# Performance work log

Hardware: AMD Instinct MI355X
Metric: run time of the kernel (lower is better)

Reference implementation:

```python
import jax, jax.numpy as jnp
import numpy as np

B, L, D, H, M = 2, 512, 1024, 16, 16384
HD = D // H  # 64


def setup_inputs() -> dict:
    key = jax.random.key(0)
    ks = jax.random.split(key, 8)
    s = 0.02
    return {
        "x": jax.random.normal(ks[0], (B, L, D), dtype=jnp.float32),
        "mem_keys": jax.random.normal(ks[1], (M, HD), dtype=jnp.float32),
        "mem_values": jax.random.normal(ks[2], (M, HD), dtype=jnp.float32),
        "Wq": jax.random.normal(ks[3], (D, D), dtype=jnp.float32) * s,
        "bq": jnp.zeros((D,), jnp.float32),
        "Wk": jax.random.normal(ks[4], (D, D), dtype=jnp.float32) * s,
        "bk": jnp.zeros((D,), jnp.float32),
        "Wv": jax.random.normal(ks[5], (D, D), dtype=jnp.float32) * s,
        "bv": jnp.zeros((D,), jnp.float32),
        "Wo": jax.random.normal(ks[6], (D, D), dtype=jnp.float32) * s,
        "bo": jnp.zeros((D,), jnp.float32),
        "top_k": 8,
    }


def reference(x, mem_keys, mem_values, Wq, bq, Wk, bk, Wv, bv, Wo, bo, top_k):
    b, l, d = x.shape
    h, hd = H, d // H
    # Q/K/V projections -> [B, L, H, HD]
    q = (x @ Wq.T + bq).reshape(b, l, h, hd)
    k = (x @ Wk.T + bk).reshape(b, l, h, hd)
    v = (x @ Wv.T + bv).reshape(b, l, h, hd)

    # exact inner-product top-k memory search (FAISS equivalent) per (b, l, h) query
    q_flat = q.reshape(b * l * h, hd)
    sim = q_flat @ mem_keys.T                      # [B*L*H, M]
    idx = jax.lax.top_k(sim, top_k)[1]             # [B*L*H, K]
    # gather retrieved KV, lay out as memory-prefix along seq: [B, L*K, H, HD]
    m_k = mem_keys[idx].reshape(b, l, h, top_k, hd).transpose(0, 1, 3, 2, 4).reshape(b, l * top_k, h, hd)
    m_v = mem_values[idx].reshape(b, l, h, top_k, hd).transpose(0, 1, 3, 2, 4).reshape(b, l * top_k, h, hd)

    k_full = jnp.concatenate([m_k, k], axis=1)     # [B, Lm+L, H, HD]
    v_full = jnp.concatenate([m_v, v], axis=1)
    lm = l * top_k

    scale = 1.0 / np.sqrt(hd)
    scores = jnp.einsum("blhd,bmhd->bhlm", q, k_full) * scale
    # memory prefix always visible; local part causal (flash_attn bottom-right causal)
    i = jnp.arange(l)[:, None]
    j = jnp.arange(lm + l)[None, :]
    mask = (j < lm) | ((j - lm) <= i)              # [L, Lm+L]
    neg = jnp.finfo(scores.dtype).min
    attn = jax.nn.softmax(jnp.where(mask, scores, neg), axis=-1)
    out = jnp.einsum("bhlm,bmhd->blhd", attn, v_full).reshape(b, l, d)
    return out @ Wo.T + bo
```

## Files before the change

kernel.cpp:

```cpp
#include <hip/hip_runtime.h>

typedef __bf16 bf16_t;
typedef __bf16 bf16x8 __attribute__((ext_vector_type(8)));
typedef __bf16 bf16x4 __attribute__((ext_vector_type(4)));
typedef __bf16 bf16x2 __attribute__((ext_vector_type(2)));
typedef float f32x4 __attribute__((ext_vector_type(4)));

#define DEV __device__ __forceinline__
#define MFMA16 __builtin_amdgcn_mfma_f32_16x16x32_bf16

constexpr int Bb = 2, Ls = 512, Dd = 1024, Hh = 16, HD = 64, Mm = 16384, TK = 8;
constexpr int KSPLIT = 4;
constexpr int CAP = 40;
constexpr int NQ = Bb * Ls * Hh;
constexpr int CH = 3;

constexpr size_t OFF_QF   = 0;
constexpr size_t OFF_KH2  = OFF_QF + (size_t)NQ * HD;
constexpr size_t OFF_KL2  = OFF_KH2 + (size_t)NQ * HD / 2;
constexpr size_t OFF_VH2  = OFF_KL2 + (size_t)NQ * HD / 2;
constexpr size_t OFF_VL2  = OFF_VH2 + (size_t)NQ * HD / 2;
constexpr size_t OFF_QH   = OFF_VL2 + (size_t)NQ * HD / 2;
constexpr size_t OFF_QL   = OFF_QH + (size_t)NQ * HD / 2;
constexpr size_t OFF_KHG  = OFF_QL + (size_t)NQ * HD / 2;
constexpr size_t OFF_FCAND = OFF_KHG + (size_t)Mm * HD / 2;
constexpr size_t OFF_FCNT  = OFF_FCAND + (size_t)KSPLIT * NQ * CAP;
constexpr size_t OFF_F8   = OFF_FCNT + (size_t)KSPLIT * NQ;
constexpr size_t OFF_ML   = OFF_F8 + (size_t)NQ * TK;
constexpr size_t OFF_PA   = OFF_ML + (size_t)CH * NQ * 2;
constexpr size_t WS_ELEMS = OFF_PA + (size_t)CH * NQ * HD + 16;
constexpr size_t WS_BYTES = WS_ELEMS * 4;

constexpr size_t OFF_GKL = OFF_FCAND;
constexpr size_t OFF_GVH = OFF_GKL + (size_t)Mm * HD / 2;
constexpr size_t OFF_GVL = OFF_GVH + (size_t)Mm * HD / 2;
static_assert(OFF_GVL + (size_t)Mm * HD / 2 <= OFF_FCNT, "alias fits in FCAND");

DEV void ld8f(const float* p, float* dst) {
  float4 a = *(const float4*)p, b = *(const float4*)(p + 4);
  dst[0]=a.x; dst[1]=a.y; dst[2]=a.z; dst[3]=a.w;
  dst[4]=b.x; dst[5]=b.y; dst[6]=b.z; dst[7]=b.w;
}

DEV void split8(const float* av, bf16x8& hi, bf16x8& lo) {
#pragma unroll
  for (int j = 0; j < 8; ++j) {
    bf16_t h_ = (bf16_t)av[j];
    hi[j] = h_;
    lo[j] = (bf16_t)(av[j] - (float)h_);
  }
}

DEV bf16x8 ld8h(const bf16_t* p) {
  bf16x4 a = *(const bf16x4*)p;
  bf16x4 b = *(const bf16x4*)(p + 4);
  bf16x8 r;
#pragma unroll
  for (int i = 0; i < 4; ++i) { r[i] = a[i]; r[i + 4] = b[i]; }
  return r;
}

__global__ __launch_bounds__(256) void ws_sentinel(float* __restrict__ out, int n, float v) {
  int i = blockIdx.x * 256 + threadIdx.x;
  if (i < n) out[i] = v;
}

__global__ __launch_bounds__(256) void prep_keys(const float* __restrict__ mk,
                                                 bf16_t* __restrict__ khg) {
  const size_t i = ((size_t)blockIdx.x * 256 + threadIdx.x) * 8;
  float v[8]; ld8f(mk + i, v);
  bf16x8 h;
#pragma unroll
  for (int j = 0; j < 8; ++j) h[j] = (bf16_t)v[j];
  *(bf16x8*)(khg + i) = h;
}

__global__ __launch_bounds__(256) void prep_kv2(const float* __restrict__ mk,
                                                const float* __restrict__ mv,
                                                bf16_t* __restrict__ gkl,
                                                bf16_t* __restrict__ gvh,
                                                bf16_t* __restrict__ gvl) {
  const size_t i = ((size_t)blockIdx.x * 256 + threadIdx.x) * 8;
  float a[8]; ld8f(mk + i, a);
  float b[8]; ld8f(mv + i, b);
  bf16x8 kl, vh, vl;
#pragma unroll
  for (int j = 0; j < 8; ++j) {
    bf16_t kh_ = (bf16_t)a[j];
    kl[j] = (bf16_t)(a[j] - (float)kh_);
    bf16_t vh_ = (bf16_t)b[j];
    vh[j] = vh_;
    vl[j] = (bf16_t)(b[j] - (float)vh_);
  }
  *(bf16x8*)(gkl + i) = kl;
  *(bf16x8*)(gvh + i) = vh;
  *(bf16x8*)(gvl + i) = vl;
}

__global__ __launch_bounds__(256) void qkv_mfma(
    const float* __restrict__ x,
    const float* __restrict__ Wq, const float* __restrict__ bq,
    const float* __restrict__ Wk, const float* __restrict__ bk,
    const float* __restrict__ Wv, const float* __restrict__ bv,
    float* __restrict__ qf, bf16_t* __restrict__ qhp, bf16_t* __restrict__ qlp,
    bf16_t* __restrict__ kh2, bf16_t* __restrict__ kl2,
    bf16_t* __restrict__ vh2, bf16_t* __restrict__ vl2) {
  __shared__ __align__(16) bf16_t WHs[2][64][40];
  __shared__ __align__(16) bf16_t WLs[2][64][40];
  const int z = blockIdx.z;
  const float* W    = (z == 0) ? Wq : ((z == 1) ? Wk : Wv);
  const float* bias = (z == 0) ? bq : ((z == 1) ? bk : bv);
  const int tid = threadIdx.x;
  const int lane = tid & 63, wv = tid >> 6;
  const int l15 = lane & 15, quad = lane >> 4;
  const int mrow = blockIdx.x * 64 + wv * 16 + l15;
  const int ncol0 = blockIdx.y * 64;
  const int srow = tid >> 2, scol = (tid & 3) * 8;
  f32x4 acc[4] = {};
  const size_t abase = (size_t)mrow * Dd + quad * 8;
  const size_t wbase = (size_t)(ncol0 + srow) * Dd + scol;
  {
    float wv8[8]; ld8f(W + wbase, wv8);
    bf16x8 h, l; split8(wv8, h, l);
    *(bf16x8*)&WHs[0][srow][scol] = h;
    *(bf16x8*)&WLs[0][srow][scol] = l;
  }
  int p = 0;
  for (int kk = 0; kk < Dd; kk += 32) {
    __syncthreads();
    if (kk + 32 < Dd) {
      float wv8[8]; ld8f(W + wbase + kk + 32, wv8);
      bf16x8 h, l; split8(wv8, h, l);
      *(bf16x8*)&WHs[p ^ 1][srow][scol] = h;
      *(bf16x8*)&WLs[p ^ 1][srow][scol] = l;
    }
    float av[8]; ld8f(x + abase + kk, av);
    bf16x8 ahi, alo; split8(av, ahi, alo);
#pragma unroll
    for (int t = 0; t < 4; ++t) {
      const bf16x8 bhi = *(const bf16x8*)&WHs[p][t * 16 + l15][quad * 8];
      const bf16x8 blo = *(const bf16x8*)&WLs[p][t * 16 + l15][quad * 8];
      acc[t] = MFMA16(ahi, bhi, acc[t], 0, 0, 0);
      acc[t] = MFMA16(alo, bhi, acc[t], 0, 0, 0);
      acc[t] = MFMA16(ahi, blo, acc[t], 0, 0, 0);
    }
    p ^= 1;
  }
#pragma unroll
  for (int t = 0; t < 4; ++t) {
    int col = ncol0 + t * 16 + l15;
    int h = col >> 6, hd = col & 63;
    float bb = bias[col];
#pragma unroll
    for (int r = 0; r < 4; ++r) {
      int row = blockIdx.x * 64 + wv * 16 + quad * 4 + r;
      int b = row >> 9, l = row & 511;
      float val = acc[t][r] + bb;
      size_t o = ((size_t)(b * Hh + h) * Ls + l) * HD + hd;
      if (z == 0) {
        qf[o] = val;
        bf16_t hv = (bf16_t)val;
        qhp[o] = hv;
        qlp[o] = (bf16_t)(val - (float)hv);
      } else {
        bf16_t hv = (bf16_t)val;
        bf16_t lv = (bf16_t)(val - (float)hv);
        if (z == 1) { kh2[o] = hv; kl2[o] = lv; }
        else        { vh2[o] = hv; vl2[o] = lv; }
      }
    }
  }
}

__global__ __launch_bounds__(256, 4) void topk_thresh(
    const bf16_t* __restrict__ qh, const bf16_t* __restrict__ khg,
    int* __restrict__ fcand, int* __restrict__ fcnt) {
  __shared__ __align__(16) float W8a[4][64][8];
  __shared__ __align__(16) float W8b[4][64][8];
  __shared__ float Tarr[64];
  __shared__ int   cntq[64];
  __shared__ int   Cand[64][CAP];

  const int tid = threadIdx.x;
  const int lane = tid & 63, w = tid >> 6;
  const int l15 = lane & 15, quad = lane >> 4;
  const int qbase = blockIdx.x * 64;
  const int split = blockIdx.y;
  const int key0 = split * (Mm / KSPLIT);
  constexpr int NT = (Mm / KSPLIT) / 64;

  bf16x8 bq[4][2];
#pragma unroll
  for (int g = 0; g < 4; ++g) {
    const bf16_t* qp = qh + (size_t)(qbase + g * 16 + l15) * HD + quad * 8;
    bq[g][0] = *(const bf16x8*)qp;
    bq[g][1] = *(const bf16x8*)(qp + 32);
  }

  const bf16_t* kbase = khg + (size_t)(key0 + w * 16 + l15) * HD + quad * 8;

  float s8g[4][8];
#pragma unroll
  for (int g = 0; g < 4; ++g)
#pragma unroll
    for (int r = 0; r < 8; ++r) s8g[g][r] = -3.0e38f;

  bf16x8 a0 = *(const bf16x8*)(kbase);
  bf16x8 a1 = *(const bf16x8*)(kbase + 32);
  for (int tile = 0; tile < NT; ++tile) {
    const bf16_t* np = kbase + (size_t)((tile + 1 < NT) ? tile + 1 : 0) * (64 * HD);
    bf16x8 n0 = *(const bf16x8*)(np);
    bf16x8 n1 = *(const bf16x8*)(np + 32);
#pragma unroll
    for (int g = 0; g < 4; ++g) {
      f32x4 acc = {0.f, 0.f, 0.f, 0.f};
      acc = MFMA16(a0, bq[g][0], acc, 0, 0, 0);
      acc = MFMA16(a1, bq[g][1], acc, 0, 0, 0);
      float m4 = fmaxf(fmaxf(acc[0], acc[1]), fmaxf(acc[2], acc[3]));
      if (m4 > s8g[g][7]) {
        s8g[g][7] = m4;
#pragma unroll
        for (int p = 7; p > 0; --p)
          if (s8g[g][p] > s8g[g][p - 1]) { float t = s8g[g][p]; s8g[g][p] = s8g[g][p - 1]; s8g[g][p - 1] = t; }
      }
    }
    a0 = n0; a1 = n1;
  }

#pragma unroll
  for (int g = 0; g < 4; ++g) {
    float part[8];
#pragma unroll
    for (int r = 0; r < 8; ++r) part[r] = __shfl_xor(s8g[g][r], 16);
    float c[8];
#pragma unroll
    for (int r = 0; r < 8; ++r) c[r] = fmaxf(s8g[g][r], part[7 - r]);
    if (quad == g) {
#pragma unroll
      for (int r = 0; r < 8; ++r) W8a[w][g * 16 + l15][r] = c[r];
    }
    if (quad == (g ^ 2)) {
#pragma unroll
      for (int r = 0; r < 8; ++r) W8b[w][g * 16 + l15][r] = c[r];
    }
  }
  __syncthreads();
  if (tid < 64) {
    float t8[8];
#pragma unroll
    for (int r = 0; r < 8; ++r) t8[r] = -3.0e38f;
#pragma unroll
    for (int wv2 = 0; wv2 < 4; ++wv2) {
#pragma unroll
      for (int half = 0; half < 2; ++half) {
        const float* src = half ? &W8b[wv2][tid][0] : &W8a[wv2][tid][0];
        float4 u0 = *(const float4*)&src[0];
        float4 u1 = *(const float4*)&src[4];
        float vals[8] = {u0.x, u0.y, u0.z, u0.w, u1.x, u1.y, u1.z, u1.w};
#pragma unroll
        for (int r = 0; r < 8; ++r) {
          float v = vals[r];
          if (v > t8[7]) {
            t8[7] = v;
#pragma unroll
            for (int p = 7; p > 0; --p)
              if (t8[p] > t8[p - 1]) { float tt = t8[p]; t8[p] = t8[p - 1]; t8[p - 1] = tt; }
          }
        }
      }
    }
    Tarr[tid] = t8[7];
    cntq[tid] = 0;
  }
  __syncthreads();
  float Tq[4];
#pragma unroll
  for (int g = 0; g < 4; ++g) Tq[g] = Tarr[g * 16 + l15];

  a0 = *(const bf16x8*)(kbase);
  a1 = *(const bf16x8*)(kbase + 32);
  for (int tile = 0; tile < NT; ++tile) {
    const bf16_t* np = kbase + (size_t)((tile + 1 < NT) ? tile + 1 : 0) * (64 * HD);
    bf16x8 n0 = *(const bf16x8*)(np);
    bf16x8 n1 = *(const bf16x8*)(np + 32);
#pragma unroll
    for (int g = 0; g < 4; ++g) {
      f32x4 acc = {0.f, 0.f, 0.f, 0.f};
      acc = MFMA16(a0, bq[g][0], acc, 0, 0, 0);
      acc = MFMA16(a1, bq[g][1], acc, 0, 0, 0);
      const int kb = key0 + tile * 64 + w * 16 + quad * 4;
      const int qq = g * 16 + l15;
#pragma unroll
      for (int r = 0; r < 4; ++r) {
        if (acc[r] >= Tq[g]) {
          int pos = atomicAdd(&cntq[qq], 1);
          if (pos < CAP) Cand[qq][pos] = kb + r;
        }
      }
    }
    a0 = n0; a1 = n1;
  }
  __syncthreads();
  if (tid < 64) {
    int c = cntq[tid];
    fcnt[(size_t)split * NQ + qbase + tid] = (c < CAP) ? c : CAP;
  }
  for (int i = tid; i < 64 * CAP; i += 256) {
    int q = i / CAP, s = i - q * CAP;
    fcand[((size_t)split * NQ + qbase + q) * CAP + s] = Cand[q][s];
  }
}

__global__ __launch_bounds__(64) void rescore8(
    const float* __restrict__ qf, const float* __restrict__ mk,
    const int* __restrict__ fcand, const int* __restrict__ fcnt,
    int* __restrict__ f8) {
  const int qid = blockIdx.x * 64 + threadIdx.x;
  float q[64];
#pragma unroll
  for (int c = 0; c < 16; ++c) {
    float4 v4 = *(const float4*)(qf + (size_t)qid * HD + 4 * c);
    q[4*c]=v4.x; q[4*c+1]=v4.y; q[4*c+2]=v4.z; q[4*c+3]=v4.w;
  }
  float sc[TK]; int id[TK];
#pragma unroll
  for (int r = 0; r < TK; ++r) { sc[r] = -3.0e38f; id[r] = 0x7fffffff; }
#pragma unroll 1
  for (int sp = 0; sp < KSPLIT; ++sp) {
    int cnt = fcnt[(size_t)sp * NQ + qid];
    if (cnt > CAP) cnt = CAP;
#pragma unroll 1
    for (int c = 0; c < cnt; ++c) {
      int kidx = fcand[((size_t)sp * NQ + qid) * CAP + c] & (Mm - 1);
      const float4* kr = (const float4*)(mk + (size_t)kidx * HD);
      float a0 = 0, a1 = 0, a2 = 0, a3 = 0;
#pragma unroll
      for (int cc = 0; cc < 16; ++cc) {
        float4 kv = kr[cc];
        a0 += q[4*cc]*kv.x; a1 += q[4*cc+1]*kv.y; a2 += q[4*cc+2]*kv.z; a3 += q[4*cc+3]*kv.w;
      }
      float s = (a0 + a1) + (a2 + a3);
      if (s > sc[TK - 1] || (s == sc[TK - 1] && kidx < id[TK - 1])) {
        sc[TK - 1] = s; id[TK - 1] = kidx;
#pragma unroll
        for (int p = TK - 1; p > 0; --p) {
          bool sw = (sc[p] > sc[p - 1]) || (sc[p] == sc[p - 1] && id[p] < id[p - 1]);
          if (sw) {
            float ts = sc[p]; sc[p] = sc[p - 1]; sc[p - 1] = ts;
            int   ti = id[p]; id[p] = id[p - 1]; id[p - 1] = ti;
          }
        }
      }
    }
  }
#pragma unroll
  for (int r = 0; r < TK; ++r) f8[(size_t)qid * TK + r] = id[r] & (Mm - 1);
}

__global__ __launch_bounds__(256) void flash_mfma(
    const bf16_t* __restrict__ qh, const bf16_t* __restrict__ ql,
    const bf16_t* __restrict__ kh2, const bf16_t* __restrict__ kl2,
    const bf16_t* __restrict__ vh2, const bf16_t* __restrict__ vl2,
    const bf16_t* __restrict__ khg, const bf16_t* __restrict__ gkl,
    const bf16_t* __restrict__ gvh, const bf16_t* __restrict__ gvl,
    const int* __restrict__ f8, float* __restrict__ ml, float* __restrict__ pacc) {
  __shared__ __align__(16) bf16_t KH[64][72];
  __shared__ __align__(16) bf16_t KL[64][72];
  __shared__ __align__(16) bf16_t VTH[64][68];
  __shared__ __align__(16) bf16_t VTL[64][68];
  __shared__ __align__(16) bf16_t PH[64][72];
  __shared__ __align__(16) bf16_t PL[64][72];

  const int tid = threadIdx.x;
  const int lane = tid & 63, w = tid >> 6;
  const int l15 = lane & 15, quad = lane >> 4;
  const int qt = blockIdx.x, bh = blockIdx.y, chunk = blockIdx.z;
  const int il = qt * 64 + w * 16 + l15;
  const int qid = bh * Ls + il;
  const bf16x8 qh0 = *(const bf16x8*)(qh + (size_t)qid * HD + quad * 8);
  const bf16x8 qh1 = *(const bf16x8*)(qh + (size_t)qid * HD + 32 + quad * 8);
  const bf16x8 ql0 = *(const bf16x8*)(ql + (size_t)qid * HD + quad * 8);
  const bf16x8 ql1 = *(const bf16x8*)(ql + (size_t)qid * HD + 32 + quad * 8);

  f32x4 O[4] = {};
  float m = -3.0e38f, lsum = 0.f;
  const float scale = 0.125f;
  const int tbase = chunk * 24;
  const int nmem  = (chunk == 2) ? 16 : 24;
  const int ntiles = (chunk == 2) ? 17 + qt : 24;
  const int skey = tid >> 2, spart = tid & 3;
  const int kpair = tid & 31, dgroup = tid >> 5;

  bf16x8 kA0, kA1, kB0, kB1;
  bf16x8 vha, vhb, vla, vlb;
  bf16x2 vth[8], vtl[8];
  auto stage_load = [&](int t) {
    const bf16_t *ksh, *ksl, *vah, *val_, *vbh, *vbl;
    if (chunk == 2 && t >= nmem) {
      int jlK = (t - nmem) * 64 + skey;
      size_t ro = ((size_t)bh * Ls + jlK) * HD + spart * 16;
      ksh = kh2 + ro; ksl = kl2 + ro;
      int jlV = (t - nmem) * 64 + 2 * kpair;
      size_t ra = ((size_t)bh * Ls + jlV) * HD + dgroup * 8;
      vah = vh2 + ra;      val_ = vl2 + ra;
      vbh = vh2 + ra + HD; vbl  = vl2 + ra + HD;
    } else {
      int jgK = (tbase + t) * 64 + skey;
      int sK = f8[((size_t)bh * Ls + (jgK >> 3)) * TK + (jgK & 7)] & (Mm - 1);
      size_t ro = (size_t)sK * HD + spart * 16;
      ksh = khg + ro; ksl = gkl + ro;
      int jgV = (tbase + t) * 64 + 2 * kpair;
      int2 s2 = *(const int2*)(f8 + ((size_t)bh * Ls + (jgV >> 3)) * TK + (jgV & 7));
      size_t ra = (size_t)(s2.x & (Mm - 1)) * HD + dgroup * 8;
      size_t rb = (size_t)(s2.y & (Mm - 1)) * HD + dgroup * 8;
      vah = gvh + ra; val_ = gvl + ra;
      vbh = gvh + rb; vbl  = gvl + rb;
    }
    kA0 = *(const bf16x8*)ksh; kA1 = *(const bf16x8*)(ksh + 8);
    kB0 = *(const bf16x8*)ksl; kB1 = *(const bf16x8*)(ksl + 8);
    vha = *(const bf16x8*)vah; vla = *(const bf16x8*)val_;
    vhb = *(const bf16x8*)vbh; vlb = *(const bf16x8*)vbl;
  };
  auto pack_v = [&]() {
#pragma unroll
    for (int j = 0; j < 8; ++j) {
      vth[j][0] = vha[j]; vth[j][1] = vhb[j];
      vtl[j][0] = vla[j]; vtl[j][1] = vlb[j];
    }
  };
  stage_load(0);
  pack_v();

  for (int tile = 0; tile < ntiles; ++tile) {
    const bool local_tile = (chunk == 2) && (tile >= nmem);
    __syncthreads();
    {
      *(bf16x8*)&KH[skey][spart * 16]     = kA0;
      *(bf16x8*)&KH[skey][spart * 16 + 8] = kA1;
      *(bf16x8*)&KL[skey][spart * 16]     = kB0;
      *(bf16x8*)&KL[skey][spart * 16 + 8] = kB1;
#pragma unroll
      for (int j = 0; j < 8; ++j) {
        *(bf16x2*)&VTH[dgroup * 8 + j][2 * kpair] = vth[j];
        *(bf16x2*)&VTL[dgroup * 8 + j][2 * kpair] = vtl[j];
      }
    }
    __syncthreads();
    if (tile + 1 < ntiles) stage_load(tile + 1);

    f32x4 S[4];
    __builtin_amdgcn_s_setprio(1);
#pragma unroll
    for (int sub = 0; sub < 4; ++sub) {
      const bf16x8 ah0 = *(const bf16x8*)&KH[sub * 16 + l15][quad * 8];
      const bf16x8 ah1 = *(const bf16x8*)&KH[sub * 16 + l15][32 + quad * 8];
      const bf16x8 al0 = *(const bf16x8*)&KL[sub * 16 + l15][quad * 8];
      const bf16x8 al1 = *(const bf16x8*)&KL[sub * 16 + l15][32 + quad * 8];
      f32x4 acc = {0.f, 0.f, 0.f, 0.f};
      acc = MFMA16(ah0, qh0, acc, 0, 0, 0);
      acc = MFMA16(ah1, qh1, acc, 0, 0, 0);
      acc = MFMA16(al0, qh0, acc, 0, 0, 0);
      acc = MFMA16(al1, qh1, acc, 0, 0, 0);
      acc = MFMA16(ah0, ql0, acc, 0, 0, 0);
      acc = MFMA16(ah1, ql1, acc, 0, 0, 0);
#pragma unroll
      for (int r = 0; r < 4; ++r) {
        float sv = acc[r] * scale;
        if (local_tile && ((tile - nmem) * 64 + sub * 16 + quad * 4 + r) > il) sv = -3.0e38f;
        S[sub][r] = sv;
      }
    }
    __builtin_amdgcn_s_setprio(0);
    float tm = -3.0e38f;
#pragma unroll
    for (int sub = 0; sub < 4; ++sub)
#pragma unroll
      for (int r = 0; r < 4; ++r) tm = fmaxf(tm, S[sub][r]);
    tm = fmaxf(tm, __shfl_xor(tm, 16));
    tm = fmaxf(tm, __shfl_xor(tm, 32));
    float mnew = fmaxf(m, tm);
    float alpha = __expf(m - mnew);
    lsum *= alpha;
#pragma unroll
    for (int t = 0; t < 4; ++t) O[t] *= alpha;
    m = mnew;
#pragma unroll
    for (int sub = 0; sub < 4; ++sub) {
      bf16_t ph4[4], pl4[4];
#pragma unroll
      for (int r = 0; r < 4; ++r) {
        float p = __expf(S[sub][r] - mnew);
        lsum += p;
        bf16_t hv = (bf16_t)p;
        ph4[r] = hv;
        pl4[r] = (bf16_t)(p - (float)hv);
      }
      *(uint2*)&PH[w * 16 + l15][sub * 16 + quad * 4] = *(uint2*)ph4;
      *(uint2*)&PL[w * 16 + l15][sub * 16 + quad * 4] = *(uint2*)pl4;
    }
    const bf16x8 ph0 = *(const bf16x8*)&PH[w * 16 + l15][quad * 8];
    const bf16x8 ph1 = *(const bf16x8*)&PH[w * 16 + l15][32 + quad * 8];
    const bf16x8 pl0 = *(const bf16x8*)&PL[w * 16 + l15][quad * 8];
    const bf16x8 pl1 = *(const bf16x8*)&PL[w * 16 + l15][32 + quad * 8];
    __builtin_amdgcn_s_setprio(1);
#pragma unroll
    for (int t = 0; t < 4; ++t) {
      const bf16x8 vh0 = ld8h(&VTH[t * 16 + l15][quad * 8]);
      const bf16x8 vh1 = ld8h(&VTH[t * 16 + l15][32 + quad * 8]);
      const bf16x8 vl0 = ld8h(&VTL[t * 16 + l15][quad * 8]);
      const bf16x8 vl1 = ld8h(&VTL[t * 16 + l15][32 + quad * 8]);
      O[t] = MFMA16(vh0, ph0, O[t], 0, 0, 0);
      O[t] = MFMA16(vh1, ph1, O[t], 0, 0, 0);
      O[t] = MFMA16(vl0, ph0, O[t], 0, 0, 0);
      O[t] = MFMA16(vl1, ph1, O[t], 0, 0, 0);
      O[t] = MFMA16(vh0, pl0, O[t], 0, 0, 0);
      O[t] = MFMA16(vh1, pl1, O[t], 0, 0, 0);
    }
    __builtin_amdgcn_s_setprio(0);
    if (tile + 1 < ntiles) pack_v();
  }
  lsum += __shfl_xor(lsum, 16);
  lsum += __shfl_xor(lsum, 32);
  if (quad == 0) {
    ml[((size_t)chunk * NQ + qid) * 2 + 0] = m;
    ml[((size_t)chunk * NQ + qid) * 2 + 1] = lsum;
  }
  float* pa = pacc + ((size_t)chunk * NQ + qid) * 64;
#pragma unroll
  for (int t = 0; t < 4; ++t) {
    float4 v4; v4.x = O[t][0]; v4.y = O[t][1]; v4.z = O[t][2]; v4.w = O[t][3];
    *(float4*)(pa + t * 16 + quad * 4) = v4;
  }
}

__global__ __launch_bounds__(256) void oproj_comb(
    const float* __restrict__ ml, const float* __restrict__ pacc,
    const float* __restrict__ Wo, const float* __restrict__ bo,
    float* __restrict__ out) {
  __shared__ __align__(16) bf16_t WHs[2][64][40];
  __shared__ __align__(16) bf16_t WLs[2][64][40];
  const int tid = threadIdx.x;
  const int lane = tid & 63, wv = tid >> 6;
  const int l15 = lane & 15, quad = lane >> 4;
  const int mrow = blockIdx.x * 64 + wv * 16 + l15;
  const int b = mrow >> 9, l = mrow & 511;
  const int ncol0 = blockIdx.y * 64;
  const int srow = tid >> 2, scol = (tid & 3) * 8;
  const size_t wbase = (size_t)(ncol0 + srow) * Dd + scol;
  f32x4 acc[4] = {};
  {
    float wv8[8]; ld8f(Wo + wbase, wv8);
    bf16x8 h, l2; split8(wv8, h, l2);
    *(bf16x8*)&WHs[0][srow][scol] = h;
    *(bf16x8*)&WLs[0][srow][scol] = l2;
  }
  int p = 0;
  for (int kk = 0; kk < Dd; kk += 32) {
    __syncthreads();
    if (kk + 32 < Dd) {
      float wv8[8]; ld8f(Wo + wbase + kk + 32, wv8);
      bf16x8 h, l2; split8(wv8, h, l2);
      *(bf16x8*)&WHs[p ^ 1][srow][scol] = h;
      *(bf16x8*)&WLs[p ^ 1][srow][scol] = l2;
    }
    const int h = kk >> 6;
    const size_t qid = (size_t)(b * Hh + h) * Ls + l;
    float m0 = ml[qid * 2 + 0],                    l0 = ml[qid * 2 + 1];
    float m1 = ml[((size_t)NQ + qid) * 2 + 0],     l1 = ml[((size_t)NQ + qid) * 2 + 1];
    float m2 = ml[((size_t)2 * NQ + qid) * 2 + 0], l2v = ml[((size_t)2 * NQ + qid) * 2 + 1];
    float M = fmaxf(m0, fmaxf(m1, m2));
    float w0 = __expf(m0 - M), w1 = __expf(m1 - M), w2 = __expf(m2 - M);
    float inv = 1.f / (w0 * l0 + w1 * l1 + w2 * l2v);
    const int d0 = (kk & 63) + quad * 8;
    float a0v[8], a1v[8], a2v[8], av[8];
    ld8f(pacc + qid * 64 + d0, a0v);
    ld8f(pacc + ((size_t)NQ + qid) * 64 + d0, a1v);
    ld8f(pacc + ((size_t)2 * NQ + qid) * 64 + d0, a2v);
#pragma unroll
    for (int j = 0; j < 8; ++j) av[j] = (w0 * a0v[j] + w1 * a1v[j] + w2 * a2v[j]) * inv;
    bf16x8 ahi, alo; split8(av, ahi, alo);
#pragma unroll
    for (int t = 0; t < 4; ++t) {
      const bf16x8 whi = *(const bf16x8*)&WHs[p][t * 16 + l15][quad * 8];
      const bf16x8 wlo = *(const bf16x8*)&WLs[p][t * 16 + l15][quad * 8];
      acc[t] = MFMA16(ahi, whi, acc[t], 0, 0, 0);
      acc[t] = MFMA16(alo, whi, acc[t], 0, 0, 0);
      acc[t] = MFMA16(ahi, wlo, acc[t], 0, 0, 0);
    }
    p ^= 1;
  }
#pragma unroll
  for (int t = 0; t < 4; ++t) {
    int col = ncol0 + t * 16 + l15;
    float bb = bo[col];
#pragma unroll
    for (int r = 0; r < 4; ++r) {
      int row = blockIdx.x * 64 + wv * 16 + quad * 4 + r;
      out[(size_t)row * Dd + col] = acc[t][r] + bb;
    }
  }
}

extern "C" void kernel_launch(void* const* d_in, const int* in_sizes, int n_in,
                              void* d_out, int out_size, void* d_ws, size_t ws_size,
                              hipStream_t stream) {
  (void)in_sizes; (void)n_in;
  const float* x  = (const float*)d_in[0];
  const float* mk = (const float*)d_in[1];
  const float* mv = (const float*)d_in[2];
  const float* Wq = (const float*)d_in[3];
  const float* bq = (const float*)d_in[4];
  const float* Wk = (const float*)d_in[5];
  const float* bk = (const float*)d_in[6];
  const float* Wv = (const float*)d_in[7];
  const float* bv = (const float*)d_in[8];
  const float* Wo = (const float*)d_in[9];
  const float* bo = (const float*)d_in[10];
  float* ws = (float*)d_ws;

  if (ws_size < WS_BYTES) {
    float v = (float)(ws_size >> 20) + 0.5f;
    ws_sentinel<<<(out_size + 255) / 256, 256, 0, stream>>>((float*)d_out, out_size, v);
    return;
  }

  float*  QF    = ws + OFF_QF;
  bf16_t* KH2   = (bf16_t*)(ws + OFF_KH2);
  bf16_t* KL2   = (bf16_t*)(ws + OFF_KL2);
  bf16_t* VH2   = (bf16_t*)(ws + OFF_VH2);
  bf16_t* VL2   = (bf16_t*)(ws + OFF_VL2);
  bf16_t* QH    = (bf16_t*)(ws + OFF_QH);
  bf16_t* QL    = (bf16_t*)(ws + OFF_QL);
  bf16_t* KHG   = (bf16_t*)(ws + OFF_KHG);
  int*    FCAND = (int*)(ws + OFF_FCAND);
  int*    FCNT  = (int*)(ws + OFF_FCNT);
  int*    F8    = (int*)(ws + OFF_F8);
  float*  ML    = ws + OFF_ML;
  float*  PA    = ws + OFF_PA;
  bf16_t* GKL   = (bf16_t*)(ws + OFF_GKL);
  bf16_t* GVH   = (bf16_t*)(ws + OFF_GVH);
  bf16_t* GVL   = (bf16_t*)(ws + OFF_GVL);

  prep_keys<<<(Mm * HD) / (256 * 8), 256, 0, stream>>>(mk, KHG);
  qkv_mfma<<<dim3(16, 16, 3), 256, 0, stream>>>(x, Wq, bq, Wk, bk, Wv, bv,
                                                QF, QH, QL, KH2, KL2, VH2, VL2);
  topk_thresh<<<dim3(NQ / 64, KSPLIT), 256, 0, stream>>>(QH, KHG, FCAND, FCNT);
  rescore8<<<NQ / 64, 64, 0, stream>>>(QF, mk, FCAND, FCNT, F8);
  prep_kv2<<<(Mm * HD) / (256 * 8), 256, 0, stream>>>(mk, mv, GKL, GVH, GVL);
  flash_mfma<<<dim3(8, 32, 3), 256, 0, stream>>>(QH, QL, KH2, KL2, VH2, VL2,
                                                 KHG, GKL, GVH, GVL, F8, ML, PA);
  oproj_comb<<<dim3(16, 16), 256, 0, stream>>>(ML, PA, Wo, bo, (float*)d_out);
}
```

Baseline: 520.6 us.

## Switch top-k threshold kernel to 32x32 MFMA with per-wave query/key split

Rewrites the top-k threshold and candidate-collection passes to use 32x32x16 bf16 MFMA instead of 16x16x32. Each wave now owns 32 queries and half of the split's key range, replacing the earlier layout where every wave covered all 64 queries across four 16-query groups. Each lane tracks a single top-8 of block maxima over 16 keys instead of four groups of 4-key maxima, which cuts per-tile compare-and-insert work and shuffles. The trade-off is coarser 16-key bucketing, which may lower the threshold and admit more candidates, raising the chance of hitting the CAP overflow limit.

```diff
diff --git a/kernel.cpp b/kernel.cpp
--- a/kernel.cpp
+++ b/kernel.cpp
@@ -5,9 +5,11 @@
 typedef __bf16 bf16x4 __attribute__((ext_vector_type(4)));
 typedef __bf16 bf16x2 __attribute__((ext_vector_type(2)));
 typedef float f32x4 __attribute__((ext_vector_type(4)));
+typedef float f32x16 __attribute__((ext_vector_type(16)));
 
 #define DEV __device__ __forceinline__
 #define MFMA16 __builtin_amdgcn_mfma_f32_16x16x32_bf16
+#define MFMA32 __builtin_amdgcn_mfma_f32_32x32x16_bf16
 
 constexpr int Bb = 2, Ls = 512, Dd = 1024, Hh = 16, HD = 64, Mm = 16384, TK = 8;
 constexpr int KSPLIT = 4;
@@ -175,85 +177,77 @@
 __global__ __launch_bounds__(256, 4) void topk_thresh(
     const bf16_t* __restrict__ qh, const bf16_t* __restrict__ khg,
     int* __restrict__ fcand, int* __restrict__ fcnt) {
-  __shared__ __align__(16) float W8a[4][64][8];
-  __shared__ __align__(16) float W8b[4][64][8];
+  __shared__ __align__(16) float W8[4][2][32][8];
   __shared__ float Tarr[64];
   __shared__ int   cntq[64];
   __shared__ int   Cand[64][CAP];
 
   const int tid = threadIdx.x;
   const int lane = tid & 63, w = tid >> 6;
-  const int l15 = lane & 15, quad = lane >> 4;
+  const int l31 = lane & 31, hi = lane >> 5;
+  const int qhalf = w & 1, keyrange = w >> 1;
   const int qbase = blockIdx.x * 64;
   const int split = blockIdx.y;
-  const int key0 = split * (Mm / KSPLIT);
-  constexpr int NT = (Mm / KSPLIT) / 64;
-
-  bf16x8 bq[4][2];
-#pragma unroll
-  for (int g = 0; g < 4; ++g) {
-    const bf16_t* qp = qh + (size_t)(qbase + g * 16 + l15) * HD + quad * 8;
-    bq[g][0] = *(const bf16x8*)qp;
-    bq[g][1] = *(const bf16x8*)(qp + 32);
-  }
-
-  const bf16_t* kbase = khg + (size_t)(key0 + w * 16 + l15) * HD + quad * 8;
-
-  float s8g[4][8];
-#pragma unroll
-  for (int g = 0; g < 4; ++g)
-#pragma unroll
-    for (int r = 0; r < 8; ++r) s8g[g][r] = -3.0e38f;
+  const int key0 = split * (Mm / KSPLIT) + keyrange * (Mm / KSPLIT / 2);
+  constexpr int NT = (Mm / KSPLIT / 2) / 32;
+  const int qq = qhalf * 32 + l31;
+
+  bf16x8 bq[4];
+#pragma unroll
+  for (int c = 0; c < 4; ++c)
+    bq[c] = *(const bf16x8*)(qh + (size_t)(qbase + qq) * HD + c * 16 + hi * 8);
+
+  const bf16_t* kbase = khg + (size_t)(key0 + l31) * HD + hi * 8;
+
+  float s8[8];
+#pragma unroll
+  for (int r = 0; r < 8; ++r) s8[r] = -3.0e38f;
 
   bf16x8 a0 = *(const bf16x8*)(kbase);
-  bf16x8 a1 = *(const bf16x8*)(kbase + 32);
+  bf16x8 a1 = *(const bf16x8*)(kbase + 16);
+  bf16x8 a2 = *(const bf16x8*)(kbase + 32);
+  bf16x8 a3 = *(const bf16x8*)(kbase + 48);
   for (int tile = 0; tile < NT; ++tile) {
-    const bf16_t* np = kbase + (size_t)((tile + 1 < NT) ? tile + 1 : 0) * (64 * HD);
+    const bf16_t* np = kbase + (size_t)((tile + 1 < NT) ? tile + 1 : 0) * (32 * HD);
     bf16x8 n0 = *(const bf16x8*)(np);
-    bf16x8 n1 = *(const bf16x8*)(np + 32);
-#pragma unroll
-    for (int g = 0; g < 4; ++g) {
-      f32x4 acc = {0.f, 0.f, 0.f, 0.f};
-      acc = MFMA16(a0, bq[g][0], acc, 0, 0, 0);
-      acc = MFMA16(a1, bq[g][1], acc, 0, 0, 0);
-      float m4 = fmaxf(fmaxf(acc[0], acc[1]), fmaxf(acc[2], acc[3]));
-      if (m4 > s8g[g][7]) {
-        s8g[g][7] = m4;
-#pragma unroll
-        for (int p = 7; p > 0; --p)
-          if (s8g[g][p] > s8g[g][p - 1]) { float t = s8g[g][p]; s8g[g][p] = s8g[g][p - 1]; s8g[g][p - 1] = t; }
-      }
-    }
-    a0 = n0; a1 = n1;
-  }
-
-#pragma unroll
-  for (int g = 0; g < 4; ++g) {
-    float part[8];
-#pragma unroll
-    for (int r = 0; r < 8; ++r) part[r] = __shfl_xor(s8g[g][r], 16);
-    float c[8];
-#pragma unroll
-    for (int r = 0; r < 8; ++r) c[r] = fmaxf(s8g[g][r], part[7 - r]);
-    if (quad == g) {
-#pragma unroll
-      for (int r = 0; r < 8; ++r) W8a[w][g * 16 + l15][r] = c[r];
-    }
-    if (quad == (g ^ 2)) {
-#pragma unroll
-      for (int r = 0; r < 8; ++r) W8b[w][g * 16 + l15][r] = c[r];
-    }
+    bf16x8 n1 = *(const bf16x8*)(np + 16);
+    bf16x8 n2 = *(const bf16x8*)(np + 32);
+    bf16x8 n3 = *(const bf16x8*)(np + 48);
+    f32x16 acc = {};
+    acc = MFMA32(a0, bq[0], acc, 0, 0, 0);
+    acc = MFMA32(a1, bq[1], acc, 0, 0, 0);
+    acc = MFMA32(a2, bq[2], acc, 0, 0, 0);
+    acc = MFMA32(a3, bq[3], acc, 0, 0, 0);
+    float p0 = fmaxf(acc[0], acc[1]),   p1 = fmaxf(acc[2], acc[3]);
+    float p2 = fmaxf(acc[4], acc[5]),   p3 = fmaxf(acc[6], acc[7]);
+    float p4 = fmaxf(acc[8], acc[9]),   p5 = fmaxf(acc[10], acc[11]);
+    float p6 = fmaxf(acc[12], acc[13]), p7 = fmaxf(acc[14], acc[15]);
+    float q0 = fmaxf(p0, p1), q1 = fmaxf(p2, p3), q2 = fmaxf(p4, p5), q3 = fmaxf(p6, p7);
+    float m16 = fmaxf(fmaxf(q0, q1), fmaxf(q2, q3));
+    if (m16 > s8[7]) {
+      s8[7] = m16;
+#pragma unroll
+      for (int p = 7; p > 0; --p)
+        if (s8[p] > s8[p - 1]) { float t = s8[p]; s8[p] = s8[p - 1]; s8[p - 1] = t; }
+    }
+    a0 = n0; a1 = n1; a2 = n2; a3 = n3;
+  }
+  {
+    float* dst = &W8[w][hi][l31][0];
+#pragma unroll
+    for (int r = 0; r < 8; ++r) dst[r] = s8[r];
   }
   __syncthreads();
   if (tid < 64) {
+    const int mqh = tid >> 5, mql = tid & 31;
     float t8[8];
 #pragma unroll
     for (int r = 0; r < 8; ++r) t8[r] = -3.0e38f;
 #pragma unroll
-    for (int wv2 = 0; wv2 < 4; ++wv2) {
-#pragma unroll
-      for (int half = 0; half < 2; ++half) {
-        const float* src = half ? &W8b[wv2][tid][0] : &W8a[wv2][tid][0];
+    for (int kr = 0; kr < 2; ++kr) {
+#pragma unroll
+      for (int h2 = 0; h2 < 2; ++h2) {
+        const float* src = &W8[kr * 2 + mqh][h2][mql][0];
         float4 u0 = *(const float4*)&src[0];
         float4 u1 = *(const float4*)&src[4];
         float vals[8] = {u0.x, u0.y, u0.z, u0.w, u1.x, u1.y, u1.z, u1.w};
@@ -273,32 +267,32 @@
     cntq[tid] = 0;
   }
   __syncthreads();
-  float Tq[4];
-#pragma unroll
-  for (int g = 0; g < 4; ++g) Tq[g] = Tarr[g * 16 + l15];
+  const float Tq = Tarr[qq];
 
   a0 = *(const bf16x8*)(kbase);
-  a1 = *(const bf16x8*)(kbase + 32);
+  a1 = *(const bf16x8*)(kbase + 16);
+  a2 = *(const bf16x8*)(kbase + 32);
+  a3 = *(const bf16x8*)(kbase + 48);
   for (int tile = 0; tile < NT; ++tile) {
-    const bf16_t* np = kbase + (size_t)((tile + 1 < NT) ? tile + 1 : 0) * (64 * HD);
+    const bf16_t* np = kbase + (size_t)((tile + 1 < NT) ? tile + 1 : 0) * (32 * HD);
     bf16x8 n0 = *(const bf16x8*)(np);
-    bf16x8 n1 = *(const bf16x8*)(np + 32);
-#pragma unroll
-    for (int g = 0; g < 4; ++g) {
-      f32x4 acc = {0.f, 0.f, 0.f, 0.f};
-      acc = MFMA16(a0, bq[g][0], acc, 0, 0, 0);
-      acc = MFMA16(a1, bq[g][1], acc, 0, 0, 0);
-      const int kb = key0 + tile * 64 + w * 16 + quad * 4;
-      const int qq = g * 16 + l15;
-#pragma unroll
-      for (int r = 0; r < 4; ++r) {
-        if (acc[r] >= Tq[g]) {
-          int pos = atomicAdd(&cntq[qq], 1);
-          if (pos < CAP) Cand[qq][pos] = kb + r;
-        }
-      }
-    }
-    a0 = n0; a1 = n1;
+    bf16x8 n1 = *(const bf16x8*)(np + 16);
+    bf16x8 n2 = *(const bf16x8*)(np + 32);
+    bf16x8 n3 = *(const bf16x8*)(np + 48);
+    f32x16 acc = {};
+    acc = MFMA32(a0, bq[0], acc, 0, 0, 0);
+    acc = MFMA32(a1, bq[1], acc, 0, 0, 0);
+    acc = MFMA32(a2, bq[2], acc, 0, 0, 0);
+    acc = MFMA32(a3, bq[3], acc, 0, 0, 0);
+    const int kb = key0 + tile * 32 + 4 * hi;
+#pragma unroll
+    for (int r = 0; r < 16; ++r) {
+      if (acc[r] >= Tq) {
+        int pos = atomicAdd(&cntq[qq], 1);
+        if (pos < CAP) Cand[qq][pos] = kb + (r & 3) + 8 * (r >> 2);
+      }
+    }
+    a0 = n0; a1 = n1; a2 = n2; a3 = n3;
   }
   __syncthreads();
   if (tid < 64) {
```

After: 629.5 us. 1.21x slower.
